# Kernel optimization log

Hardware: AMD Instinct MI355X
Metric: run time of the kernel (lower is better)

The kernel has to match this reference:

```python
import jax, jax.numpy as jnp
import numpy as np

N = 50000   # nodes
E = 400000  # edges
IN_DIM, H1, H2, OUT_DIM = 512, 256, 62, 128


def _param(key, shape, scale=0.05):
    return jax.random.normal(key, shape, dtype=jnp.float32) * scale


def setup_inputs() -> dict:
    key = jax.random.key(0)
    ks = jax.random.split(key, 24)
    x = jax.random.normal(ks[0], (N, IN_DIM), dtype=jnp.float32)
    edge_index_neg = jax.random.randint(ks[1], (2, E), 0, N, dtype=jnp.int64)
    d = {
        "x": x, "edge_index_neg": edge_index_neg,
        # nn.Linear params (W stored as [in, out])
        "W1": _param(ks[2], (IN_DIM, H1)), "b1": _param(ks[3], (H1,)),
        "W2": _param(ks[4], (H1, H2)),    "b2": _param(ks[5], (H2,)),
        "W3": _param(ks[6], (H2, OUT_DIM)), "b3": _param(ks[7], (OUT_DIM,)),
        # GCNConv params: lin weight (no bias) + post-aggregation bias
        "Wg1": _param(ks[8], (H1, H1)),   "bg1": _param(ks[9], (H1,)),
        "Wg2": _param(ks[10], (H2, H2)),  "bg2": _param(ks[11], (H2,)),
        "Wg3": _param(ks[12], (OUT_DIM, OUT_DIM)), "bg3": _param(ks[13], (OUT_DIM,)),
        "Wg4": _param(ks[14], (OUT_DIM, OUT_DIM)), "bg4": _param(ks[15], (OUT_DIM,)),
        "Wg5": _param(ks[16], (OUT_DIM, OUT_DIM)), "bg5": _param(ks[17], (OUT_DIM,)),
        "Wg6": _param(ks[18], (OUT_DIM, OUT_DIM)), "bg6": _param(ks[19], (OUT_DIM,)),
    }
    return d


def _build_norm(edge_index):
    # PyG GCNConv: add self-loops, symmetric normalization D^-1/2 A D^-1/2
    loop = jnp.arange(N, dtype=edge_index.dtype)
    src = jnp.concatenate([edge_index[0], loop])
    dst = jnp.concatenate([edge_index[1], loop])
    deg = jax.ops.segment_sum(jnp.ones_like(dst, dtype=jnp.float32), dst, num_segments=N)
    dinv = jnp.where(deg > 0, jax.lax.rsqrt(jnp.maximum(deg, 1.0)), 0.0)
    norm = dinv[src] * dinv[dst]  # [E+N]
    return src, dst, norm


def _gcn(x, W, b, src, dst, norm):
    h = x @ W                                   # [N, F]
    msg = h[src] * norm[:, None]                # gather + edge scale
    out = jax.ops.segment_sum(msg, dst, num_segments=N)  # scatter-add
    return out + b


def reference(x, edge_index_neg, W1, b1, W2, b2, W3, b3,
              Wg1, bg1, Wg2, bg2, Wg3, bg3, Wg4, bg4, Wg5, bg5, Wg6, bg6):
    src, dst, norm = _build_norm(edge_index_neg)
    relu = jax.nn.relu
    x1l = x @ W1 + b1
    x1 = x1l + relu(_gcn(x1l, Wg1, bg1, src, dst, norm))
    x2l = x1 @ W2 + b2
    x2 = x2l + relu(_gcn(x2l, Wg2, bg2, src, dst, norm))
    x3l = x2 @ W3 + b3
    x3 = x3l + 0.5 * relu(_gcn(x3l, Wg3, bg3, src, dst, norm))
    x4 = x3 + 0.5 * relu(_gcn(x4_in := x3, Wg4, bg4, src, dst, norm))
    x5 = x4 + 0.25 * relu(_gcn(x4, Wg5, bg5, src, dst, norm))
    x6 = x5 + 0.25 * _gcn(x5, Wg6, bg6, src, dst, norm)
    return x6
```

## Files before the change

kernel.cpp:

```cpp
#include <hip/hip_runtime.h>

#define NN 50000
#define NE 400000
#define NBLK 196

using short8 = __attribute__((ext_vector_type(8))) short;
using f32x4  = __attribute__((ext_vector_type(4))) float;
using u16x2  = __attribute__((ext_vector_type(2))) unsigned short;
using u16x4  = __attribute__((ext_vector_type(4))) unsigned short;

__device__ __forceinline__ unsigned short f2b(float f) {
    union { float f; unsigned int u; } x; x.f = f;
    unsigned int u = x.u;
    u += 0x7fffu + ((u >> 16) & 1u);
    return (unsigned short)(u >> 16);
}
__device__ __forceinline__ float b2f(unsigned short u) {
    union { unsigned int u; float f; } x; x.u = ((unsigned int)u) << 16;
    return x.f;
}

#define SWZ(b, row) ((b) ^ (((row) & 7) << 4))

__global__ __launch_bounds__(256) void zero2_k(int* a, int* b) {
    int i = blockIdx.x * 256 + threadIdx.x;
    if (i < NN) { a[i] = 0; b[i] = 0; }
}
__global__ __launch_bounds__(256) void count_k(const int* __restrict__ dst, int* __restrict__ indeg) {
    int e = blockIdx.x * 256 + threadIdx.x;
    if (e < NE) atomicAdd(&indeg[dst[e]], 1);
}
__global__ __launch_bounds__(256) void dinv_k(const int* __restrict__ indeg, float* __restrict__ dinv) {
    int i = blockIdx.x * 256 + threadIdx.x;
    if (i < NN) dinv[i] = rsqrtf((float)(1 + indeg[i]));
}
__global__ __launch_bounds__(256) void scan1_k(const int* __restrict__ indeg, int* __restrict__ tmp,
                                               int* __restrict__ bsum) {
    __shared__ int s[256];
    int t = threadIdx.x, i = blockIdx.x * 256 + t;
    int v = (i < NN) ? indeg[i] : 0;
    s[t] = v; __syncthreads();
    for (int off = 1; off < 256; off <<= 1) {
        int x = (t >= off) ? s[t - off] : 0;
        __syncthreads();
        s[t] += x;
        __syncthreads();
    }
    if (i < NN) tmp[i] = s[t];
    if (t == 255) bsum[blockIdx.x] = s[255];
}
__global__ __launch_bounds__(256) void scan2_k(const int* __restrict__ bsum, int* __restrict__ boff) {
    __shared__ int s[256];
    int t = threadIdx.x;
    int v = (t < NBLK) ? bsum[t] : 0;
    s[t] = v; __syncthreads();
    for (int off = 1; off < 256; off <<= 1) {
        int x = (t >= off) ? s[t - off] : 0;
        __syncthreads();
        s[t] += x;
        __syncthreads();
    }
    if (t < NBLK) boff[t] = s[t] - v;
}
__global__ __launch_bounds__(256) void scan3_k(const int* __restrict__ tmp, const int* __restrict__ indeg,
                                               const int* __restrict__ boff, int* __restrict__ rowptr) {
    int i = blockIdx.x * 256 + threadIdx.x;
    if (i < NN) rowptr[i] = tmp[i] - indeg[i] + boff[i >> 8];
    if (i == 0) rowptr[NN] = NE;
}
__global__ __launch_bounds__(256) void fill_k(const int* __restrict__ src, const int* __restrict__ dst,
                                              const float* __restrict__ dinv, const int* __restrict__ rowptr,
                                              int* __restrict__ cursor, int2* __restrict__ ebn) {
    int e = blockIdx.x * 256 + threadIdx.x;
    if (e >= NE) return;
    int s = src[e], d = dst[e];
    int pos = atomicAdd(&cursor[d], 1);
    ebn[rowptr[d] + pos] = make_int2(s, __float_as_int(dinv[s] * dinv[d]));
}

struct WSegs {
    const float* W[9];
    unsigned short* Wt[9];
    int K[9], N[9], Kp[9];
    int c0[10];
};
__global__ __launch_bounds__(256) void wcast_all_k(WSegs s) {
    int blk = blockIdx.x;
    #pragma unroll
    for (int g = 0; g < 9; g++) {
        if (blk >= s.c0[g] && blk < s.c0[g + 1]) {
            int idx = (blk - s.c0[g]) * 256 + threadIdx.x;
            int Kp = s.Kp[g];
            int n = idx / Kp, k = idx % Kp;
            float v = (n < s.N[g] && k < s.K[g]) ? s.W[g][(size_t)k * s.N[g] + n] : 0.0f;
            s.Wt[g][idx] = f2b(v);
        }
    }
}

template<bool AF32, int BM, int BN>
__global__ __launch_bounds__(256) void gemm_mfma_k(
    const void* __restrict__ Araw, const unsigned short* __restrict__ Bt,
    const float* __restrict__ bias, unsigned short* __restrict__ C,
    int M, int lda, int Kp, int N, int ldc) {
    constexpr int MR = BM / 32;
    constexpr int NF = BN / 32;
    constexpr int nA = BM / 32;
    constexpr int nB = BN / 32;
    __shared__ __align__(16) char lds[BM * 128 + BN * 128];
    char* AsB = lds;
    char* BsB = lds + BM * 128;

    int tid = threadIdx.x;
    int lane = tid & 63, wave = tid >> 6;
    int wr = wave >> 1, wc = wave & 1;
    int lr = lane & 15, lk = lane >> 4;
    int r0 = blockIdx.x * BM, c0 = blockIdx.y * BN;

    f32x4 acc[MR][NF];
    #pragma unroll
    for (int m = 0; m < MR; m++)
        #pragma unroll
        for (int n = 0; n < NF; n++)
            acc[m][n] = (f32x4){0.f, 0.f, 0.f, 0.f};

    float4 fa0[nA], fa1[nA];
    short8 ra[nA], rb[nB];

    auto LOAD = [&](int k0) {
        #pragma unroll
        for (int c = 0; c < nA; c++) {
            int o = tid + c * 256, row = o >> 3, oct = o & 7;
            int gr = r0 + row;
            if constexpr (AF32) {
                if (gr < M) {
                    const float* p = (const float*)Araw + (size_t)gr * lda + k0 + oct * 8;
                    fa0[c] = *(const float4*)p;
                    fa1[c] = *(const float4*)(p + 4);
                } else {
                    fa0[c] = make_float4(0, 0, 0, 0);
                    fa1[c] = make_float4(0, 0, 0, 0);
                }
            } else {
                short8 z = {0, 0, 0, 0, 0, 0, 0, 0};
                ra[c] = (gr < M)
                    ? *(const short8*)((const unsigned short*)Araw + (size_t)gr * lda + k0 + oct * 8)
                    : z;
            }
        }
        #pragma unroll
        for (int c = 0; c < nB; c++) {
            int o = tid + c * 256, row = o >> 3, oct = o & 7;
            rb[c] = *(const short8*)(Bt + (size_t)(c0 + row) * Kp + k0 + oct * 8);
        }
    };
    auto STORE = [&]() {
        #pragma unroll
        for (int c = 0; c < nA; c++) {
            int o = tid + c * 256, row = o >> 3, oct = o & 7;
            short8 v;
            if constexpr (AF32) {
                v[0] = (short)f2b(fa0[c].x); v[1] = (short)f2b(fa0[c].y);
                v[2] = (short)f2b(fa0[c].z); v[3] = (short)f2b(fa0[c].w);
                v[4] = (short)f2b(fa1[c].x); v[5] = (short)f2b(fa1[c].y);
                v[6] = (short)f2b(fa1[c].z); v[7] = (short)f2b(fa1[c].w);
            } else {
                v = ra[c];
            }
            *(short8*)(AsB + SWZ(row * 128 + oct * 16, row)) = v;
        }
        #pragma unroll
        for (int c = 0; c < nB; c++) {
            int o = tid + c * 256, row = o >> 3, oct = o & 7;
            *(short8*)(BsB + SWZ(row * 128 + oct * 16, row)) = rb[c];
        }
    };

    int nt = Kp >> 6;
    LOAD(0);
    STORE();
    __syncthreads();
    for (int t = 0; t < nt; t++) {
        if (t + 1 < nt) LOAD((t + 1) << 6);
        #pragma unroll
        for (int kk = 0; kk < 2; kk++) {
            int kb = kk * 64 + lk * 16;
            short8 a[MR], b[NF];
            #pragma unroll
            for (int m = 0; m < MR; m++) {
                int row = wr * (BM / 2) + m * 16 + lr;
                a[m] = *(short8*)(AsB + SWZ(row * 128 + kb, row));
            }
            #pragma unroll
            for (int n = 0; n < NF; n++) {
                int row = wc * (BN / 2) + n * 16 + lr;
                b[n] = *(short8*)(BsB + SWZ(row * 128 + kb, row));
            }
            #pragma unroll
            for (int m = 0; m < MR; m++)
                #pragma unroll
                for (int n = 0; n < NF; n++)
                    acc[m][n] = __builtin_amdgcn_mfma_f32_16x16x32_bf16(a[m], b[n], acc[m][n], 0, 0, 0);
        }
        __syncthreads();
        if (t + 1 < nt) { STORE(); __syncthreads(); }
    }

    unsigned short* ldsC = (unsigned short*)lds;
    #pragma unroll
    for (int n = 0; n < NF; n++) {
        int cc = wc * (BN / 2) + n * 16 + lr;
        int gc = c0 + cc;
        float bv = (bias != nullptr && gc < N) ? bias[gc] : 0.0f;
        bool ok = gc < N;
        #pragma unroll
        for (int m = 0; m < MR; m++)
            #pragma unroll
            for (int j = 0; j < 4; j++) {
                int row = wr * (BM / 2) + m * 16 + lk * 4 + j;
                float v = ok ? acc[m][n][j] + bv : 0.0f;
                ldsC[row * BN + cc] = f2b(v);
            }
    }
    __syncthreads();
    constexpr int CH = (BM * BN) / 2048;
    #pragma unroll
    for (int c = 0; c < CH; c++) {
        int o = tid + c * 256;
        int row = o / (BN / 8), col = (o % (BN / 8)) * 8;
        int gr = r0 + row;
        if (gr < M)
            *(short8*)(C + (size_t)gr * ldc + c0 + col) = *(short8*)(ldsC + row * BN + col);
    }
}

template<int VEC> struct BV;
template<> struct BV<1> { using T = unsigned short; };
template<> struct BV<2> { using T = u16x2; };
template<> struct BV<4> { using T = u16x4; };

template<int VEC, bool OUTF32>
__global__ __launch_bounds__(256) void gather_k(
    const unsigned short* __restrict__ h, const unsigned short* __restrict__ base,
    const float* __restrict__ dinv, const float* __restrict__ bias,
    const int2* __restrict__ ebn, const int* __restrict__ rowptr,
    void* __restrict__ outraw, float alpha, int dorelu, int F) {
    const int ld = 64 * VEC;
    int w = (blockIdx.x * 256 + threadIdx.x) >> 6;
    int lane = threadIdx.x & 63;
    if (w >= NN) return;
    using LT = typename BV<VEC>::T;

    float acc[VEC];
    float dn = dinv[w];
    {
        LT t = *(const LT*)(h + (size_t)w * ld + lane * VEC);
        const unsigned short* tu = (const unsigned short*)&t;
        #pragma unroll
        for (int v = 0; v < VEC; v++) acc[v] = b2f(tu[v]) * dn * dn;
    }
    int e = rowptr[w], end = rowptr[w + 1];
    for (; e + 4 <= end; e += 4) {
        int2 q0 = ebn[e], q1 = ebn[e + 1], q2 = ebn[e + 2], q3 = ebn[e + 3];
        LT t0 = *(const LT*)(h + (size_t)q0.x * ld + lane * VEC);
        LT t1 = *(const LT*)(h + (size_t)q1.x * ld + lane * VEC);
        LT t2 = *(const LT*)(h + (size_t)q2.x * ld + lane * VEC);
        LT t3 = *(const LT*)(h + (size_t)q3.x * ld + lane * VEC);
        float n0 = __int_as_float(q0.y), n1 = __int_as_float(q1.y);
        float n2 = __int_as_float(q2.y), n3 = __int_as_float(q3.y);
        const unsigned short* u0 = (const unsigned short*)&t0;
        const unsigned short* u1 = (const unsigned short*)&t1;
        const unsigned short* u2 = (const unsigned short*)&t2;
        const unsigned short* u3 = (const unsigned short*)&t3;
        #pragma unroll
        for (int v = 0; v < VEC; v++)
            acc[v] += b2f(u0[v]) * n0 + b2f(u1[v]) * n1 + b2f(u2[v]) * n2 + b2f(u3[v]) * n3;
    }
    for (; e < end; e++) {
        int2 q0 = ebn[e];
        LT t0 = *(const LT*)(h + (size_t)q0.x * ld + lane * VEC);
        float n0 = __int_as_float(q0.y);
        const unsigned short* u0 = (const unsigned short*)&t0;
        #pragma unroll
        for (int v = 0; v < VEC; v++) acc[v] += b2f(u0[v]) * n0;
    }
    LT bt = *(const LT*)(base + (size_t)w * ld + lane * VEC);
    const unsigned short* bu = (const unsigned short*)&bt;
    #pragma unroll
    for (int v = 0; v < VEC; v++) {
        int f = lane * VEC + v;
        float a = acc[v] + ((f < F) ? bias[f] : 0.0f);
        if (dorelu) a = fmaxf(a, 0.0f);
        float res = (f < F) ? b2f(bu[v]) + alpha * a : 0.0f;
        if (OUTF32) ((float*)outraw)[(size_t)w * ld + f] = res;
        else        ((unsigned short*)outraw)[(size_t)w * ld + f] = f2b(res);
    }
}

extern "C" void kernel_launch(void* const* d_in, const int* in_sizes, int n_in,
                              void* d_out, int out_size, void* d_ws, size_t ws_size,
                              hipStream_t stream) {
    const float* x   = (const float*)d_in[0];
    const int*   ei  = (const int*)d_in[1];
    const float* W1  = (const float*)d_in[2];  const float* b1  = (const float*)d_in[3];
    const float* W2  = (const float*)d_in[4];  const float* b2  = (const float*)d_in[5];
    const float* W3  = (const float*)d_in[6];  const float* b3  = (const float*)d_in[7];
    const float* Wg1 = (const float*)d_in[8];  const float* bg1 = (const float*)d_in[9];
    const float* Wg2 = (const float*)d_in[10]; const float* bg2 = (const float*)d_in[11];
    const float* Wg3 = (const float*)d_in[12]; const float* bg3 = (const float*)d_in[13];
    const float* Wg4 = (const float*)d_in[14]; const float* bg4 = (const float*)d_in[15];
    const float* Wg5 = (const float*)d_in[16]; const float* bg5 = (const float*)d_in[17];
    const float* Wg6 = (const float*)d_in[18]; const float* bg6 = (const float*)d_in[19];
    const int* srcv = ei;
    const int* dstv = ei + NE;

    float* dinv = (float*)d_ws;
    unsigned short* hA = (unsigned short*)(dinv + 51200);
    unsigned short* hB = hA + (size_t)NN * 256;
    unsigned short* hC = hB + (size_t)NN * 256;
    unsigned short* W1t  = hC + (size_t)NN * 256;
    unsigned short* Wg1t = W1t  + 256 * 512;
    unsigned short* W2t  = Wg1t + 256 * 256;
    unsigned short* Wg2t = W2t  + 64 * 256;
    unsigned short* W3t  = Wg2t + 64 * 64;
    unsigned short* Wg3t = W3t  + 128 * 64;
    unsigned short* Wg4t = Wg3t + 128 * 128;
    unsigned short* Wg5t = Wg4t + 128 * 128;
    unsigned short* Wg6t = Wg5t + 128 * 128;
    int* indeg  = (int*)(Wg6t + 128 * 128);
    int* cursor = indeg + 51200;
    int* tmp    = cursor + 51200;
    int* rowptr = tmp + 51200;
    int* bsum   = rowptr + 51264;
    int* boff   = bsum + 256;
    int2* ebn   = (int2*)(boff + 256);

    zero2_k<<<NBLK, 256, 0, stream>>>(indeg, cursor);
    count_k<<<(NE + 255) / 256, 256, 0, stream>>>(dstv, indeg);
    dinv_k<<<NBLK, 256, 0, stream>>>(indeg, dinv);
    scan1_k<<<NBLK, 256, 0, stream>>>(indeg, tmp, bsum);
    scan2_k<<<1, 256, 0, stream>>>(bsum, boff);
    scan3_k<<<NBLK, 256, 0, stream>>>(tmp, indeg, boff, rowptr);
    fill_k<<<(NE + 255) / 256, 256, 0, stream>>>(srcv, dstv, dinv, rowptr, cursor, ebn);

    {
        WSegs s;
        const float* Ws[9] = {W1, Wg1, W2, Wg2, W3, Wg3, Wg4, Wg5, Wg6};
        unsigned short* Wts[9] = {W1t, Wg1t, W2t, Wg2t, W3t, Wg3t, Wg4t, Wg5t, Wg6t};
        int Ks[9]  = {512, 256, 256, 62, 62, 128, 128, 128, 128};
        int Ns[9]  = {256, 256, 62, 62, 128, 128, 128, 128, 128};
        int Kps[9] = {512, 256, 256, 64, 64, 128, 128, 128, 128};
        int Nps[9] = {256, 256, 64, 64, 128, 128, 128, 128, 128};
        int c = 0;
        for (int g = 0; g < 9; g++) {
            s.W[g] = Ws[g]; s.Wt[g] = Wts[g];
            s.K[g] = Ks[g]; s.N[g] = Ns[g]; s.Kp[g] = Kps[g];
            s.c0[g] = c;
            c += (Kps[g] * Nps[g]) / 256;
        }
        s.c0[9] = c;
        wcast_all_k<<<c, 256, 0, stream>>>(s);
    }

    const int GX = (NN + 63) / 64;
    const int GG = (NN * 64 + 255) / 256;

    gemm_mfma_k<true, 64, 128><<<dim3(GX, 2), 256, 0, stream>>>(x, W1t, b1, hA, NN, 512, 512, 256, 256);
    gemm_mfma_k<false, 64, 128><<<dim3(GX, 2), 256, 0, stream>>>(hA, Wg1t, nullptr, hB, NN, 256, 256, 256, 256);
    gather_k<4, false><<<GG, 256, 0, stream>>>(hB, hA, dinv, bg1, ebn, rowptr, hC, 1.0f, 1, 256);
    gemm_mfma_k<false, 64, 64><<<dim3(GX, 1), 256, 0, stream>>>(hC, W2t, b2, hA, NN, 256, 256, 62, 64);
    gemm_mfma_k<false, 64, 64><<<dim3(GX, 1), 256, 0, stream>>>(hA, Wg2t, nullptr, hB, NN, 64, 64, 62, 64);
    gather_k<1, false><<<GG, 256, 0, stream>>>(hB, hA, dinv, bg2, ebn, rowptr, hC, 1.0f, 1, 62);
    gemm_mfma_k<false, 64, 128><<<dim3(GX, 1), 256, 0, stream>>>(hC, W3t, b3, hA, NN, 64, 64, 128, 128);
    gemm_mfma_k<false, 64, 128><<<dim3(GX, 1), 256, 0, stream>>>(hA, Wg3t, nullptr, hB, NN, 128, 128, 128, 128);
    gather_k<2, false><<<GG, 256, 0, stream>>>(hB, hA, dinv, bg3, ebn, rowptr, hC, 0.5f, 1, 128);
    gemm_mfma_k<false, 64, 128><<<dim3(GX, 1), 256, 0, stream>>>(hC, Wg4t, nullptr, hA, NN, 128, 128, 128, 128);
    gather_k<2, false><<<GG, 256, 0, stream>>>(hA, hC, dinv, bg4, ebn, rowptr, hB, 0.5f, 1, 128);
    gemm_mfma_k<false, 64, 128><<<dim3(GX, 1), 256, 0, stream>>>(hB, Wg5t, nullptr, hA, NN, 128, 128, 128, 128);
    gather_k<2, false><<<GG, 256, 0, stream>>>(hA, hB, dinv, bg5, ebn, rowptr, hC, 0.25f, 1, 128);
    gemm_mfma_k<false, 64, 128><<<dim3(GX, 1), 256, 0, stream>>>(hC, Wg6t, nullptr, hA, NN, 128, 128, 128, 128);
    gather_k<2, true><<<GG, 256, 0, stream>>>(hA, hC, dinv, bg6, ebn, rowptr, d_out, 0.25f, 0, 128);
}
```

Measured before the change: 383.5 us.

## Double-buffer GEMM LDS, pad C staging, unroll gather by 8, fuse dinv into scan

Four separate changes. The GEMM now double-buffers its shared-memory tiles, so one barrier per K-step replaces two and the next tile is stored while the current one is used. The C staging buffer gets a padded row stride. The CSR aggregation loop issues eight neighbor loads per iteration instead of four, giving more memory-level parallelism. The dinv computation is folded into scan3, removing one kernel launch. In exchange, double buffering doubles LDS use, which may lower occupancy, and the wider unroll raises register pressure.

```diff
diff --git a/kernel.cpp b/kernel.cpp
--- a/kernel.cpp
+++ b/kernel.cpp
@@ -29,10 +29,6 @@
 __global__ __launch_bounds__(256) void count_k(const int* __restrict__ dst, int* __restrict__ indeg) {
     int e = blockIdx.x * 256 + threadIdx.x;
     if (e < NE) atomicAdd(&indeg[dst[e]], 1);
-}
-__global__ __launch_bounds__(256) void dinv_k(const int* __restrict__ indeg, float* __restrict__ dinv) {
-    int i = blockIdx.x * 256 + threadIdx.x;
-    if (i < NN) dinv[i] = rsqrtf((float)(1 + indeg[i]));
 }
 __global__ __launch_bounds__(256) void scan1_k(const int* __restrict__ indeg, int* __restrict__ tmp,
                                                int* __restrict__ bsum) {
@@ -63,9 +59,13 @@
     if (t < NBLK) boff[t] = s[t] - v;
 }
 __global__ __launch_bounds__(256) void scan3_k(const int* __restrict__ tmp, const int* __restrict__ indeg,
-                                               const int* __restrict__ boff, int* __restrict__ rowptr) {
+                                               const int* __restrict__ boff, int* __restrict__ rowptr,
+                                               float* __restrict__ dinv) {
     int i = blockIdx.x * 256 + threadIdx.x;
-    if (i < NN) rowptr[i] = tmp[i] - indeg[i] + boff[i >> 8];
+    if (i < NN) {
+        rowptr[i] = tmp[i] - indeg[i] + boff[i >> 8];
+        dinv[i] = rsqrtf((float)(1 + indeg[i]));
+    }
     if (i == 0) rowptr[NN] = NE;
 }
 __global__ __launch_bounds__(256) void fill_k(const int* __restrict__ src, const int* __restrict__ dst,
@@ -107,9 +107,8 @@
     constexpr int NF = BN / 32;
     constexpr int nA = BM / 32;
     constexpr int nB = BN / 32;
-    __shared__ __align__(16) char lds[BM * 128 + BN * 128];
-    char* AsB = lds;
-    char* BsB = lds + BM * 128;
+    constexpr int BUFB = (BM + BN) * 128;
+    __shared__ __align__(16) char lds[2 * BUFB];
 
     int tid = threadIdx.x;
     int lane = tid & 63, wave = tid >> 6;
@@ -154,7 +153,7 @@
             rb[c] = *(const short8*)(Bt + (size_t)(c0 + row) * Kp + k0 + oct * 8);
         }
     };
-    auto STORE = [&]() {
+    auto STORE = [&](char* AsB, char* BsB) {
         #pragma unroll
         for (int c = 0; c < nA; c++) {
             int o = tid + c * 256, row = o >> 3, oct = o & 7;
@@ -178,10 +177,14 @@
 
     int nt = Kp >> 6;
     LOAD(0);
-    STORE();
+    STORE(lds, lds + BM * 128);
     __syncthreads();
     for (int t = 0; t < nt; t++) {
+        char* cur = lds + (t & 1) * BUFB;
+        char* alt = lds + ((t + 1) & 1) * BUFB;
         if (t + 1 < nt) LOAD((t + 1) << 6);
+        char* AsB = cur;
+        char* BsB = cur + BM * 128;
         #pragma unroll
         for (int kk = 0; kk < 2; kk++) {
             int kb = kk * 64 + lk * 16;
@@ -202,10 +205,11 @@
                 for (int n = 0; n < NF; n++)
                     acc[m][n] = __builtin_amdgcn_mfma_f32_16x16x32_bf16(a[m], b[n], acc[m][n], 0, 0, 0);
         }
-        __syncthreads();
-        if (t + 1 < nt) { STORE(); __syncthreads(); }
-    }
-
+        if (t + 1 < nt) STORE(alt, alt + BM * 128);
+        __syncthreads();
+    }
+
+    constexpr int LDC = BN + 8;
     unsigned short* ldsC = (unsigned short*)lds;
     #pragma unroll
     for (int n = 0; n < NF; n++) {
@@ -219,7 +223,7 @@
             for (int j = 0; j < 4; j++) {
                 int row = wr * (BM / 2) + m * 16 + lk * 4 + j;
                 float v = ok ? acc[m][n][j] + bv : 0.0f;
-                ldsC[row * BN + cc] = f2b(v);
+                ldsC[row * LDC + cc] = f2b(v);
             }
     }
     __syncthreads();
@@ -230,7 +234,7 @@
         int row = o / (BN / 8), col = (o % (BN / 8)) * 8;
         int gr = r0 + row;
         if (gr < M)
-            *(short8*)(C + (size_t)gr * ldc + c0 + col) = *(short8*)(ldsC + row * BN + col);
+            *(short8*)(C + (size_t)gr * ldc + c0 + col) = *(short8*)(ldsC + row * LDC + col);
     }
 }
 
@@ -260,23 +264,32 @@
         for (int v = 0; v < VEC; v++) acc[v] = b2f(tu[v]) * dn * dn;
     }
     int e = rowptr[w], end = rowptr[w + 1];
-    for (; e + 4 <= end; e += 4) {
-        int2 q0 = ebn[e], q1 = ebn[e + 1], q2 = ebn[e + 2], q3 = ebn[e + 3];
+    for (; e + 8 <= end; e += 8) {
+        int2 q[8];
+        #pragma unroll
+        for (int i = 0; i < 8; i++) q[i] = ebn[e + i];
+        LT t[8];
+        #pragma unroll
+        for (int i = 0; i < 8; i++) t[i] = *(const LT*)(h + (size_t)q[i].x * ld + lane * VEC);
+        #pragma unroll
+        for (int i = 0; i < 8; i++) {
+            float nr = __int_as_float(q[i].y);
+            const unsigned short* u = (const unsigned short*)&t[i];
+            #pragma unroll
+            for (int v = 0; v < VEC; v++) acc[v] += b2f(u[v]) * nr;
+        }
+    }
+    for (; e + 2 <= end; e += 2) {
+        int2 q0 = ebn[e], q1 = ebn[e + 1];
         LT t0 = *(const LT*)(h + (size_t)q0.x * ld + lane * VEC);
         LT t1 = *(const LT*)(h + (size_t)q1.x * ld + lane * VEC);
-        LT t2 = *(const LT*)(h + (size_t)q2.x * ld + lane * VEC);
-        LT t3 = *(const LT*)(h + (size_t)q3.x * ld + lane * VEC);
         float n0 = __int_as_float(q0.y), n1 = __int_as_float(q1.y);
-        float n2 = __int_as_float(q2.y), n3 = __int_as_float(q3.y);
         const unsigned short* u0 = (const unsigned short*)&t0;
         const unsigned short* u1 = (const unsigned short*)&t1;
-        const unsigned short* u2 = (const unsigned short*)&t2;
-        const unsigned short* u3 = (const unsigned short*)&t3;
-        #pragma unroll
-        for (int v = 0; v < VEC; v++)
-            acc[v] += b2f(u0[v]) * n0 + b2f(u1[v]) * n1 + b2f(u2[v]) * n2 + b2f(u3[v]) * n3;
-    }
-    for (; e < end; e++) {
+        #pragma unroll
+        for (int v = 0; v < VEC; v++) acc[v] += b2f(u0[v]) * n0 + b2f(u1[v]) * n1;
+    }
+    if (e < end) {
         int2 q0 = ebn[e];
         LT t0 = *(const LT*)(h + (size_t)q0.x * ld + lane * VEC);
         float n0 = __int_as_float(q0.y);
@@ -337,10 +350,9 @@
 
     zero2_k<<<NBLK, 256, 0, stream>>>(indeg, cursor);
     count_k<<<(NE + 255) / 256, 256, 0, stream>>>(dstv, indeg);
-    dinv_k<<<NBLK, 256, 0, stream>>>(indeg, dinv);
     scan1_k<<<NBLK, 256, 0, stream>>>(indeg, tmp, bsum);
     scan2_k<<<1, 256, 0, stream>>>(bsum, boff);
-    scan3_k<<<NBLK, 256, 0, stream>>>(tmp, indeg, boff, rowptr);
+    scan3_k<<<NBLK, 256, 0, stream>>>(tmp, indeg, boff, rowptr, dinv);
     fill_k<<<(NE + 255) / 256, 256, 0, stream>>>(srcv, dstv, dinv, rowptr, cursor, ebn);
 
     {
```

Measured after the change: 383.1 us. Within noise of the previous version (-0.1%).
